# Performance work log

Measured on AMD Instinct MI355X. Metric: run time of the kernel, lower is better.

The kernel has to match this reference:

```python
import jax, jax.numpy as jnp
import numpy as np

M, N, B, L = 512, 2048, 4, 20
H_DENSITY = 0.02  # Tanner graph sparsity: row weight ~N*p=40, col weight ~M*p=10


def setup_inputs() -> dict:
    key = jax.random.key(0)
    ks = jax.random.split(key, 10)
    H = jax.random.bernoulli(ks[0], H_DENSITY, (M, N)).astype(jnp.float32)
    llrs = jax.random.uniform(ks[1], (N,), jnp.float32)
    syndromes = jax.random.randint(ks[2], (B, M, 1), 0, 2, jnp.int32)
    errors = jax.random.randint(ks[3], (B, N), 0, 2, jnp.int32)
    weights_de = jax.random.uniform(ks[4], (L, M, N), jnp.float32)
    weights_llr = jax.random.uniform(ks[5], (L, N), jnp.float32)
    marg_weights_de = jax.random.uniform(ks[6], (L, M, N), jnp.float32)
    marg_weights_llr = jax.random.uniform(ks[7], (L, N), jnp.float32)
    rhos = jnp.ones((L,), jnp.float32)
    residual_weights = jnp.zeros((L,), jnp.float32)
    return dict(syndromes=syndromes, errors=errors, H=H, llrs=llrs,
                weights_de=weights_de, weights_llr=weights_llr,
                marg_weights_de=marg_weights_de, marg_weights_llr=marg_weights_llr,
                rhos=rhos, residual_weights=residual_weights)


def reference(syndromes, errors, H, llrs, weights_de, weights_llr,
              marg_weights_de, marg_weights_llr, rhos, residual_weights):
    batch = syndromes.shape[0]
    m, n = H.shape
    rhos_norm = jax.nn.softmax(rhos)                       # (L,)
    sign = 1.0 - 2.0 * syndromes.astype(H.dtype)           # (B,m,1): (-1)**syndrome
    err_f = errors.astype(H.dtype)                         # (B,n)
    eps = 1e-6

    def step(msgs_dn, xs):
        w_de, w_llr, mw_de, mw_llr, rho, rw = xs
        # error-node (variable) update: column-sum minus self, masked by H
        msgs_en = (H * (llrs * w_llr)
                   + jnp.sum(msgs_dn * w_de, axis=1, keepdims=True)) * H - msgs_dn
        # detector-node (check) update: tanh-product rule with self-exclusion
        d = jnp.tanh(msgs_en * 0.5)
        d = jnp.where(d == 0, jnp.asarray(1.0, d.dtype), d)
        d = jnp.clip(d, -1.0 + eps, 1.0 - eps)
        row_prod = jnp.prod(d, axis=2, keepdims=True)      # (B,m,1)
        msgs_new = 2.0 * jnp.arctanh(row_prod / d) * (sign * H) + rw * msgs_dn
        # marginal beliefs and weighted BCE loss
        beliefs = jnp.sum(msgs_new * mw_de, axis=1) + llrs * mw_llr   # (B,n)
        loss_b = jnp.sum(jax.nn.softplus(beliefs) - (1.0 - err_f) * beliefs, axis=1)
        return msgs_new, rho * loss_b

    init = jnp.zeros((batch, m, n), H.dtype)
    _, losses = jax.lax.scan(
        step, init,
        (weights_de, weights_llr, marg_weights_de, marg_weights_llr,
         rhos_norm, residual_weights))
    return jnp.sum(losses) / batch
```

## Files before the change

### kernel.cpp

```cpp
#include <hip/hip_runtime.h>

#define MM 512
#define NN 2048
#define BB 4
#define LL 20
#define MAXDEG 128
#define EMAX  24576
#define NT    1024
#define RR    8
#define ROWSB 64
#define EPTB  4
#define COLSB 256
#define EPSV  1e-6f

#define WS_ROW_DEG   0
#define WS_ROW_PAD   2048
#define WS_ROW_OFFF  264192
#define WS_ROW_PTR   266240
#define WS_EDGE_CSR  268416
#define WS_WDE_G     366720
#define WS_MWDE_G    2332800
#define WS_COLPART   4298880
#define WS_BELPART   4561024
#define WS_BAR       4823168

__global__ __launch_bounds__(64)
void build_rows(const float* __restrict__ H, int* __restrict__ row_deg,
                int* __restrict__ row_pad, float* __restrict__ row_offf) {
    int i = blockIdx.x, lane = threadIdx.x;
    const float* hrow = H + (size_t)i * NN;
    int base = 0;
    for (int chunk = 0; chunk < NN / 64; ++chunk) {
        int c = chunk * 64 + lane;
        bool pred = hrow[c] != 0.0f;
        unsigned long long mask = __ballot(pred);
        int before = __popcll(mask & ((1ull << lane) - 1ull));
        if (pred) {
            int idx = base + before;
            if (idx < MAXDEG) row_pad[i * MAXDEG + idx] = c;
        }
        base += __popcll(mask);
    }
    if (lane == 0) {
        row_deg[i] = base < MAXDEG ? base : MAXDEG;
        row_offf[i] = powf(1.0f - EPSV, (float)(NN - base));
    }
}

__global__ __launch_bounds__(512)
void scan_rows(const int* __restrict__ row_deg, int* __restrict__ row_ptr) {
    __shared__ int tmp[512];
    int t = threadIdx.x;
    tmp[t] = row_deg[t];
    __syncthreads();
    for (int off = 1; off < 512; off <<= 1) {
        int v = (t >= off) ? tmp[t - off] : 0;
        __syncthreads();
        tmp[t] += v;
        __syncthreads();
    }
    if (t == 0) row_ptr[0] = 0;
    row_ptr[t + 1] = tmp[t];
}

__global__ __launch_bounds__(64)
void fill_csr(const int* __restrict__ row_deg, const int* __restrict__ row_pad,
              const int* __restrict__ row_ptr, unsigned* __restrict__ edge_csr) {
    int i = blockIdx.x, lane = threadIdx.x;
    int deg = row_deg[i], base = row_ptr[i];
    for (int k = lane; k < deg; k += 64)
        edge_csr[base + k] = ((unsigned)i << 16) | (unsigned)row_pad[i * MAXDEG + k];
}

__global__ __launch_bounds__(256)
void gather_weights(const float* __restrict__ w_de, const float* __restrict__ mw_de,
                    const unsigned* __restrict__ edge_csr, const int* __restrict__ row_ptr,
                    float* __restrict__ wde_g, float* __restrict__ mwde_g) {
    int idx = blockIdx.x * 256 + threadIdx.x;
    int l = idx / EMAX, e = idx - l * EMAX;
    if (e < row_ptr[MM]) {
        unsigned pk = edge_csr[e];
        size_t src = (size_t)l * MM * NN + (size_t)(pk >> 16) * NN + (pk & 0xffffu);
        wde_g[idx]  = w_de[src];
        mwde_g[idx] = mw_de[src];
    } else {
        wde_g[idx]  = 0.0f;
        mwde_g[idx] = 0.0f;
    }
}

__device__ __forceinline__ void grid_barrier(int* ctr) {
    __syncthreads();
    if (threadIdx.x == 0) {
        __threadfence();
        __hip_atomic_fetch_add(ctr, 1, __ATOMIC_RELAXED, __HIP_MEMORY_SCOPE_AGENT);
        while (__hip_atomic_load(ctr, __ATOMIC_RELAXED, __HIP_MEMORY_SCOPE_AGENT) < RR)
            __builtin_amdgcn_s_sleep(1);
        __threadfence();
    }
    __syncthreads();
}

__global__ __launch_bounds__(NT, 4)
void nbp_main(const int* __restrict__ synd, const int* __restrict__ errs,
              const float* __restrict__ llrs,
              const float* __restrict__ w_llr, const float* __restrict__ mw_llr,
              const float* __restrict__ rhos, const float* __restrict__ resw,
              const int* __restrict__ row_ptr, const float* __restrict__ row_offf,
              const unsigned* __restrict__ edge_csr,
              const float* __restrict__ wde_g, const float* __restrict__ mwde_g,
              float* __restrict__ colpart, float* __restrict__ belpart,
              int* __restrict__ bar, float* __restrict__ out) {
    __shared__ float d_sb[EPTB * NT];
    __shared__ float colsum_s[NN];
    __shared__ float bel_s[NN];
    __shared__ float llrs_s[NN];
    __shared__ float rowprod_s[ROWSB];
    __shared__ float rp_coef[ROWSB];
    __shared__ int   rowptr_s[ROWSB + 1];
    __shared__ float rho_n[LL];
    __shared__ float red[16];

    const int blk = blockIdx.x;
    const int b = blk & 3, r = blk >> 2;
    const int i0 = r * ROWSB;
    const int tid = threadIdx.x;
    const int lane = tid & 63, wave = tid >> 6;

    float* colpart_b = colpart + (size_t)b * RR * NN;
    float* belpart_b = belpart + (size_t)b * RR * NN;
    int*   bar_b     = bar + b * 64;
    int    bi = 0;

    if (tid == 0) {
        float mx = -1e30f;
        for (int l = 0; l < LL; ++l) mx = fmaxf(mx, rhos[l]);
        float s = 0.0f;
        for (int l = 0; l < LL; ++l) { float e = __expf(rhos[l] - mx); rho_n[l] = e; s += e; }
        for (int l = 0; l < LL; ++l) rho_n[l] /= s;
    }
    if (tid < ROWSB) {
        int i = i0 + tid;
        rowptr_s[tid] = row_ptr[i];
        rp_coef[tid] = row_offf[i] * (1.0f - 2.0f * (float)synd[b * MM + i]);
    }
    if (tid == ROWSB) rowptr_s[ROWSB] = row_ptr[i0 + ROWSB];
    for (int j = tid; j < NN; j += NT) llrs_s[j] = llrs[j];
    __syncthreads();

    const int e_lo = rowptr_s[0], e_hi = rowptr_s[ROWSB];
    const int ebase = e_lo + tid;

    unsigned idx[EPTB];
    float msg[EPTB], wv[EPTB], mv[EPTB], wvn[EPTB], d_r[EPTB];
    #pragma unroll
    for (int k = 0; k < EPTB; ++k) {
        int e = ebase + k * NT;
        int eld = e < e_hi ? e : e_lo;
        idx[k] = edge_csr[eld] - ((unsigned)i0 << 16);
        msg[k] = 0.0f;
        wv[k] = 0.0f; wvn[k] = 0.0f;
    }

    float loss = 0.0f;

    for (int l = 0; l < LL; ++l) {
        const float rw = resw[l];

        if (l == 0) {
            const float* wl = w_llr;
            for (int j = tid; j < NN; j += NT) colsum_s[j] = llrs_s[j] * wl[j];
            __syncthreads();
        } else {
            #pragma unroll
            for (int k = 0; k < EPTB; ++k) {
                if (ebase + k * NT < e_hi)
                    atomicAdd(&colsum_s[idx[k] & 0xffffu], msg[k] * wv[k]);
            }
            __syncthreads();
            for (int j = tid; j < NN; j += NT) colpart_b[r * NN + j] = colsum_s[j];
            grid_barrier(&bar_b[bi]); ++bi;
            const float* wl = w_llr + l * NN;
            for (int j = tid; j < NN; j += NT) {
                float s = llrs_s[j] * wl[j];
                const float* cp = colpart_b + j;
                #pragma unroll
                for (int r2 = 0; r2 < RR; ++r2) s += cp[r2 * NN];
                colsum_s[j] = s;
            }
            __syncthreads();
        }

        {
            const float* mwl = mwde_g + (size_t)l * EMAX;
            #pragma unroll
            for (int k = 0; k < EPTB; ++k) {
                int e = ebase + k * NT;
                mv[k] = mwl[e < EMAX ? e : EMAX - 1];
            }
        }
        #pragma unroll
        for (int k = 0; k < EPTB; ++k) {
            int j = idx[k] & 0xffffu;
            float en = colsum_s[j] - msg[k];
            float t = __expf(en);
            float d = 1.0f - 2.0f * __builtin_amdgcn_rcpf(t + 1.0f);
            if (d == 0.0f) d = 1.0f;
            d = fminf(fmaxf(d, -1.0f + EPSV), 1.0f - EPSV);
            d_r[k] = d;
            if (ebase + k * NT < e_hi) d_sb[tid + k * NT] = d;
        }
        __syncthreads();

        if (tid < ROWSB) {
            int s = rowptr_s[tid] - e_lo;
            int deg = rowptr_s[tid + 1] - rowptr_s[tid];
            float p0 = 1.0f, p1 = 1.0f, p2 = 1.0f, p3 = 1.0f;
            int c = 0;
            for (; c + 3 < deg; c += 4) {
                p0 *= d_sb[s + c];     p1 *= d_sb[s + c + 1];
                p2 *= d_sb[s + c + 2]; p3 *= d_sb[s + c + 3];
            }
            for (; c < deg; ++c) p0 *= d_sb[s + c];
            rowprod_s[tid] = p0 * p1 * p2 * p3 * rp_coef[tid];
        } else {
            for (int j = tid - ROWSB; j < NN; j += NT - ROWSB) {
                bel_s[j] = 0.0f;
                colsum_s[j] = 0.0f;
            }
        }
        __syncthreads();

        if (l + 1 < LL) {
            const float* wl = wde_g + (size_t)(l + 1) * EMAX;
            #pragma unroll
            for (int k = 0; k < EPTB; ++k) {
                int e = ebase + k * NT;
                wvn[k] = wl[e < EMAX ? e : EMAX - 1];
            }
        }
        #pragma unroll
        for (int k = 0; k < EPTB; ++k) {
            int il = idx[k] >> 16;
            int j  = idx[k] & 0xffffu;
            float rq = rowprod_s[il] * __builtin_amdgcn_rcpf(d_r[k]);
            float v = __logf(1.0f + rq) - __logf(1.0f - rq) + rw * msg[k];
            msg[k] = v;
            if (ebase + k * NT < e_hi) atomicAdd(&bel_s[j], v * mv[k]);
        }
        __syncthreads();
        for (int j = tid; j < NN; j += NT) belpart_b[r * NN + j] = bel_s[j];
        grid_barrier(&bar_b[bi]); ++bi;

        if (tid < COLSB) {
            int j = r * COLSB + tid;
            float bel = llrs_s[j] * mw_llr[l * NN + j];
            const float* bp = belpart_b + j;
            #pragma unroll
            for (int r2 = 0; r2 < RR; ++r2) bel += bp[r2 * NN];
            float sp = fmaxf(bel, 0.0f) + log1pf(__expf(-fabsf(bel)));
            loss += rho_n[l] * (sp - (1.0f - (float)errs[b * NN + j]) * bel);
        }
        #pragma unroll
        for (int k = 0; k < EPTB; ++k) wv[k] = wvn[k];
    }

    #pragma unroll
    for (int off = 32; off > 0; off >>= 1) loss += __shfl_down(loss, off);
    if (lane == 0) red[wave] = loss;
    __syncthreads();
    if (wave == 0) {
        float v = (lane < 16) ? red[lane] : 0.0f;
        #pragma unroll
        for (int off = 8; off > 0; off >>= 1) v += __shfl_down(v, off);
        if (lane == 0) atomicAdd(out, v * 0.25f);
    }
}

extern "C" void kernel_launch(void* const* d_in, const int* in_sizes, int n_in,
                              void* d_out, int out_size, void* d_ws, size_t ws_size,
                              hipStream_t stream) {
    const int*   synd  = (const int*)  d_in[0];
    const int*   errs  = (const int*)  d_in[1];
    const float* H     = (const float*)d_in[2];
    const float* llrs  = (const float*)d_in[3];
    const float* w_de  = (const float*)d_in[4];
    const float* w_llr = (const float*)d_in[5];
    const float* mw_de = (const float*)d_in[6];
    const float* mw_llr= (const float*)d_in[7];
    const float* rhos  = (const float*)d_in[8];
    const float* resw  = (const float*)d_in[9];

    char* ws = (char*)d_ws;
    int*      row_deg  = (int*)     (ws + WS_ROW_DEG);
    int*      row_pad  = (int*)     (ws + WS_ROW_PAD);
    float*    row_offf = (float*)   (ws + WS_ROW_OFFF);
    int*      row_ptr  = (int*)     (ws + WS_ROW_PTR);
    unsigned* edge_csr = (unsigned*)(ws + WS_EDGE_CSR);
    float*    wde_g    = (float*)   (ws + WS_WDE_G);
    float*    mwde_g   = (float*)   (ws + WS_MWDE_G);
    float*    colpart  = (float*)   (ws + WS_COLPART);
    float*    belpart  = (float*)   (ws + WS_BELPART);
    int*      bar      = (int*)     (ws + WS_BAR);
    float*    out      = (float*)d_out;

    hipMemsetAsync(bar, 0, BB * 64 * sizeof(int), stream);
    hipMemsetAsync(d_out, 0, sizeof(float), stream);

    build_rows<<<MM, 64, 0, stream>>>(H, row_deg, row_pad, row_offf);
    scan_rows<<<1, 512, 0, stream>>>(row_deg, row_ptr);
    fill_csr<<<MM, 64, 0, stream>>>(row_deg, row_pad, row_ptr, edge_csr);
    gather_weights<<<(LL * EMAX) / 256, 256, 0, stream>>>(w_de, mw_de, edge_csr,
                                                          row_ptr, wde_g, mwde_g);
    nbp_main<<<BB * RR, NT, 0, stream>>>(synd, errs, llrs, w_llr, mw_llr, rhos, resw,
                                         row_ptr, row_offf, edge_csr, wde_g, mwde_g,
                                         colpart, belpart, bar, out);
}
```

Baseline: 484.2 us.

## Merge column-sum exchange into belief barrier, halving grid barriers per layer

The next layer's weighted column-sum partials are now accumulated in the same pass as the belief partials and published before a single grid barrier per layer, replacing the two barriers used before. Partial buffers are double-buffered by layer parity so the next layer's writes cannot overwrite data other blocks are still reading. Edge weights are repacked per row-block slot so each thread loads four contiguous edges as float4. The row product is also split across four threads per row with shuffles. The cost is more workspace, an extra shared array, and an assumption that each row-block holds at most 4096 edges.

```diff
diff --git a/kernel.cpp b/kernel.cpp
--- a/kernel.cpp
+++ b/kernel.cpp
@@ -9,7 +9,7 @@
 #define NT    1024
 #define RR    8
 #define ROWSB 64
-#define EPTB  4
+#define SLOTS 4096
 #define COLSB 256
 #define EPSV  1e-6f
 
@@ -18,11 +18,11 @@
 #define WS_ROW_OFFF  264192
 #define WS_ROW_PTR   266240
 #define WS_EDGE_CSR  268416
-#define WS_WDE_G     366720
-#define WS_MWDE_G    2332800
-#define WS_COLPART   4298880
-#define WS_BELPART   4561024
-#define WS_BAR       4823168
+#define WS_WDE_P     366720
+#define WS_MWDE_P    2988160
+#define WS_COLPART   5609600
+#define WS_BELPART   6133888
+#define WS_BAR       6658176
 
 __global__ __launch_bounds__(64)
 void build_rows(const float* __restrict__ H, int* __restrict__ row_deg,
@@ -75,17 +75,20 @@
 __global__ __launch_bounds__(256)
 void gather_weights(const float* __restrict__ w_de, const float* __restrict__ mw_de,
                     const unsigned* __restrict__ edge_csr, const int* __restrict__ row_ptr,
-                    float* __restrict__ wde_g, float* __restrict__ mwde_g) {
+                    float* __restrict__ wde_p, float* __restrict__ mwde_p) {
     int idx = blockIdx.x * 256 + threadIdx.x;
-    int l = idx / EMAX, e = idx - l * EMAX;
-    if (e < row_ptr[MM]) {
+    int l = idx / (RR * SLOTS);
+    int rem = idx - l * (RR * SLOTS);
+    int r = rem / SLOTS, s = rem - r * SLOTS;
+    int e = row_ptr[r * ROWSB] + s;
+    if (e < row_ptr[(r + 1) * ROWSB]) {
         unsigned pk = edge_csr[e];
         size_t src = (size_t)l * MM * NN + (size_t)(pk >> 16) * NN + (pk & 0xffffu);
-        wde_g[idx]  = w_de[src];
-        mwde_g[idx] = mw_de[src];
+        wde_p[idx]  = w_de[src];
+        mwde_p[idx] = mw_de[src];
     } else {
-        wde_g[idx]  = 0.0f;
-        mwde_g[idx] = 0.0f;
+        wde_p[idx]  = 0.0f;
+        mwde_p[idx] = 0.0f;
     }
 }
 
@@ -108,12 +111,13 @@
               const float* __restrict__ rhos, const float* __restrict__ resw,
               const int* __restrict__ row_ptr, const float* __restrict__ row_offf,
               const unsigned* __restrict__ edge_csr,
-              const float* __restrict__ wde_g, const float* __restrict__ mwde_g,
+              const float* __restrict__ wde_p, const float* __restrict__ mwde_p,
               float* __restrict__ colpart, float* __restrict__ belpart,
               int* __restrict__ bar, float* __restrict__ out) {
-    __shared__ float d_sb[EPTB * NT];
+    __shared__ float d_sb[SLOTS];
     __shared__ float colsum_s[NN];
     __shared__ float bel_s[NN];
+    __shared__ float ncs_s[NN];
     __shared__ float llrs_s[NN];
     __shared__ float rowprod_s[ROWSB];
     __shared__ float rp_coef[ROWSB];
@@ -127,10 +131,7 @@
     const int tid = threadIdx.x;
     const int lane = tid & 63, wave = tid >> 6;
 
-    float* colpart_b = colpart + (size_t)b * RR * NN;
-    float* belpart_b = belpart + (size_t)b * RR * NN;
-    int*   bar_b     = bar + b * 64;
-    int    bi = 0;
+    int* bar_b = bar + b * 64;
 
     if (tid == 0) {
         float mx = -1e30f;
@@ -145,62 +146,43 @@
         rp_coef[tid] = row_offf[i] * (1.0f - 2.0f * (float)synd[b * MM + i]);
     }
     if (tid == ROWSB) rowptr_s[ROWSB] = row_ptr[i0 + ROWSB];
-    for (int j = tid; j < NN; j += NT) llrs_s[j] = llrs[j];
-    __syncthreads();
-
-    const int e_lo = rowptr_s[0], e_hi = rowptr_s[ROWSB];
-    const int ebase = e_lo + tid;
-
-    unsigned idx[EPTB];
-    float msg[EPTB], wv[EPTB], mv[EPTB], wvn[EPTB], d_r[EPTB];
+    for (int j = tid; j < NN; j += NT) {
+        float lj = llrs[j];
+        llrs_s[j] = lj;
+        colsum_s[j] = lj * w_llr[j];
+    }
+
+    const int e_lo = row_ptr[i0], e_hi = row_ptr[i0 + ROWSB];
+    const int cnt = e_hi - e_lo;
+    const int s0 = 4 * tid;
+
+    unsigned idx[4];
+    float msg[4], d_r[4];
     #pragma unroll
-    for (int k = 0; k < EPTB; ++k) {
-        int e = ebase + k * NT;
-        int eld = e < e_hi ? e : e_lo;
-        idx[k] = edge_csr[eld] - ((unsigned)i0 << 16);
+    for (int k = 0; k < 4; ++k) {
+        int e = e_lo + s0 + k;
+        idx[k] = edge_csr[(s0 + k) < cnt ? e : e_lo] - ((unsigned)i0 << 16);
         msg[k] = 0.0f;
-        wv[k] = 0.0f; wvn[k] = 0.0f;
-    }
+    }
+    __syncthreads();
 
     float loss = 0.0f;
 
     for (int l = 0; l < LL; ++l) {
         const float rw = resw[l];
-
-        if (l == 0) {
-            const float* wl = w_llr;
-            for (int j = tid; j < NN; j += NT) colsum_s[j] = llrs_s[j] * wl[j];
-            __syncthreads();
-        } else {
-            #pragma unroll
-            for (int k = 0; k < EPTB; ++k) {
-                if (ebase + k * NT < e_hi)
-                    atomicAdd(&colsum_s[idx[k] & 0xffffu], msg[k] * wv[k]);
-            }
-            __syncthreads();
-            for (int j = tid; j < NN; j += NT) colpart_b[r * NN + j] = colsum_s[j];
-            grid_barrier(&bar_b[bi]); ++bi;
-            const float* wl = w_llr + l * NN;
-            for (int j = tid; j < NN; j += NT) {
-                float s = llrs_s[j] * wl[j];
-                const float* cp = colpart_b + j;
-                #pragma unroll
-                for (int r2 = 0; r2 < RR; ++r2) s += cp[r2 * NN];
-                colsum_s[j] = s;
-            }
-            __syncthreads();
-        }
-
-        {
-            const float* mwl = mwde_g + (size_t)l * EMAX;
-            #pragma unroll
-            for (int k = 0; k < EPTB; ++k) {
-                int e = ebase + k * NT;
-                mv[k] = mwl[e < EMAX ? e : EMAX - 1];
-            }
-        }
+        const int par = l & 1;
+        float* colpart_b = colpart + ((size_t)par * BB + b) * RR * NN;
+        float* belpart_b = belpart + ((size_t)par * BB + b) * RR * NN;
+
+        const float4 mq = *(const float4*)(mwde_p + ((size_t)(l * RR + r) * SLOTS) + s0);
+        float4 wq = make_float4(0.f, 0.f, 0.f, 0.f);
+        if (l + 1 < LL)
+            wq = *(const float4*)(wde_p + ((size_t)((l + 1) * RR + r) * SLOTS) + s0);
+        const float mv[4] = {mq.x, mq.y, mq.z, mq.w};
+        const float wn[4] = {wq.x, wq.y, wq.z, wq.w};
+
         #pragma unroll
-        for (int k = 0; k < EPTB; ++k) {
+        for (int k = 0; k < 4; ++k) {
             int j = idx[k] & 0xffffu;
             float en = colsum_s[j] - msg[k];
             float t = __expf(en);
@@ -208,49 +190,45 @@
             if (d == 0.0f) d = 1.0f;
             d = fminf(fmaxf(d, -1.0f + EPSV), 1.0f - EPSV);
             d_r[k] = d;
-            if (ebase + k * NT < e_hi) d_sb[tid + k * NT] = d;
-        }
-        __syncthreads();
-
-        if (tid < ROWSB) {
-            int s = rowptr_s[tid] - e_lo;
-            int deg = rowptr_s[tid + 1] - rowptr_s[tid];
-            float p0 = 1.0f, p1 = 1.0f, p2 = 1.0f, p3 = 1.0f;
-            int c = 0;
-            for (; c + 3 < deg; c += 4) {
-                p0 *= d_sb[s + c];     p1 *= d_sb[s + c + 1];
-                p2 *= d_sb[s + c + 2]; p3 *= d_sb[s + c + 3];
+        }
+        *(float4*)&d_sb[s0] = make_float4(d_r[0], d_r[1], d_r[2], d_r[3]);
+        __syncthreads();
+
+        if (tid < 4 * ROWSB) {
+            int i = tid >> 2, q = tid & 3;
+            int s = rowptr_s[i] - e_lo;
+            int deg = rowptr_s[i + 1] - rowptr_s[i];
+            float p = 1.0f;
+            for (int c = q; c < deg; c += 4) p *= d_sb[s + c];
+            p *= __shfl_xor(p, 1);
+            p *= __shfl_xor(p, 2);
+            if (q == 0) rowprod_s[i] = p * rp_coef[i];
+        } else {
+            for (int j = tid - 4 * ROWSB; j < NN; j += NT - 4 * ROWSB) {
+                bel_s[j] = 0.0f;
+                ncs_s[j] = 0.0f;
             }
-            for (; c < deg; ++c) p0 *= d_sb[s + c];
-            rowprod_s[tid] = p0 * p1 * p2 * p3 * rp_coef[tid];
-        } else {
-            for (int j = tid - ROWSB; j < NN; j += NT - ROWSB) {
-                bel_s[j] = 0.0f;
-                colsum_s[j] = 0.0f;
-            }
-        }
-        __syncthreads();
-
-        if (l + 1 < LL) {
-            const float* wl = wde_g + (size_t)(l + 1) * EMAX;
-            #pragma unroll
-            for (int k = 0; k < EPTB; ++k) {
-                int e = ebase + k * NT;
-                wvn[k] = wl[e < EMAX ? e : EMAX - 1];
-            }
-        }
+        }
+        __syncthreads();
+
         #pragma unroll
-        for (int k = 0; k < EPTB; ++k) {
+        for (int k = 0; k < 4; ++k) {
             int il = idx[k] >> 16;
             int j  = idx[k] & 0xffffu;
             float rq = rowprod_s[il] * __builtin_amdgcn_rcpf(d_r[k]);
             float v = __logf(1.0f + rq) - __logf(1.0f - rq) + rw * msg[k];
             msg[k] = v;
-            if (ebase + k * NT < e_hi) atomicAdd(&bel_s[j], v * mv[k]);
-        }
-        __syncthreads();
-        for (int j = tid; j < NN; j += NT) belpart_b[r * NN + j] = bel_s[j];
-        grid_barrier(&bar_b[bi]); ++bi;
+            if (s0 + k < cnt) {
+                atomicAdd(&bel_s[j], v * mv[k]);
+                if (l + 1 < LL) atomicAdd(&ncs_s[j], v * wn[k]);
+            }
+        }
+        __syncthreads();
+        for (int j = tid; j < NN; j += NT) {
+            belpart_b[r * NN + j] = bel_s[j];
+            colpart_b[r * NN + j] = ncs_s[j];
+        }
+        grid_barrier(&bar_b[l]);
 
         if (tid < COLSB) {
             int j = r * COLSB + tid;
@@ -261,8 +239,17 @@
             float sp = fmaxf(bel, 0.0f) + log1pf(__expf(-fabsf(bel)));
             loss += rho_n[l] * (sp - (1.0f - (float)errs[b * NN + j]) * bel);
         }
-        #pragma unroll
-        for (int k = 0; k < EPTB; ++k) wv[k] = wvn[k];
+        if (l + 1 < LL) {
+            const float* wl_next = w_llr + (l + 1) * NN;
+            for (int j = tid; j < NN; j += NT) {
+                float s = llrs_s[j] * wl_next[j];
+                const float* cp = colpart_b + j;
+                #pragma unroll
+                for (int r2 = 0; r2 < RR; ++r2) s += cp[r2 * NN];
+                colsum_s[j] = s;
+            }
+        }
+        __syncthreads();
     }
 
     #pragma unroll
@@ -297,8 +284,8 @@
     float*    row_offf = (float*)   (ws + WS_ROW_OFFF);
     int*      row_ptr  = (int*)     (ws + WS_ROW_PTR);
     unsigned* edge_csr = (unsigned*)(ws + WS_EDGE_CSR);
-    float*    wde_g    = (float*)   (ws + WS_WDE_G);
-    float*    mwde_g   = (float*)   (ws + WS_MWDE_G);
+    float*    wde_p    = (float*)   (ws + WS_WDE_P);
+    float*    mwde_p   = (float*)   (ws + WS_MWDE_P);
     float*    colpart  = (float*)   (ws + WS_COLPART);
     float*    belpart  = (float*)   (ws + WS_BELPART);
     int*      bar      = (int*)     (ws + WS_BAR);
@@ -310,9 +297,9 @@
     build_rows<<<MM, 64, 0, stream>>>(H, row_deg, row_pad, row_offf);
     scan_rows<<<1, 512, 0, stream>>>(row_deg, row_ptr);
     fill_csr<<<MM, 64, 0, stream>>>(row_deg, row_pad, row_ptr, edge_csr);
-    gather_weights<<<(LL * EMAX) / 256, 256, 0, stream>>>(w_de, mw_de, edge_csr,
-                                                          row_ptr, wde_g, mwde_g);
+    gather_weights<<<(LL * RR * SLOTS) / 256, 256, 0, stream>>>(w_de, mw_de, edge_csr,
+                                                                row_ptr, wde_p, mwde_p);
     nbp_main<<<BB * RR, NT, 0, stream>>>(synd, errs, llrs, w_llr, mw_llr, rhos, resw,
-                                         row_ptr, row_offf, edge_csr, wde_g, mwde_g,
+                                         row_ptr, row_offf, edge_csr, wde_p, mwde_p,
                                          colpart, belpart, bar, out);
 }
```

Measured after the change: 453.3 us. 1.07x faster.
